# Performance work log

Measured on AMD Instinct MI355X. Metric: run time of the kernel, lower is better.

The kernel has to match this reference:

```python
import jax, jax.numpy as jnp
import numpy as np

D_MODEL = 1024
NUM_HEADS = 16
D_K = D_MODEL // NUM_HEADS


def setup_inputs() -> dict:
    key = jax.random.key(0)
    ks = jax.random.split(key, 11)
    B, S, D = 2, 2048, D_MODEL
    scale = 1.0 / np.sqrt(D)
    inp = {
        'q': jax.random.normal(ks[0], (B, S, D), jnp.float32),
        'k': jax.random.normal(ks[1], (B, S, D), jnp.float32),
        'v': jax.random.normal(ks[2], (B, S, D), jnp.float32),
        'wq': jax.random.normal(ks[3], (D, D), jnp.float32) * scale,
        'bq': jnp.zeros((D,), jnp.float32),
        'wk': jax.random.normal(ks[4], (D, D), jnp.float32) * scale,
        'bk': jnp.zeros((D,), jnp.float32),
        'wv': jax.random.normal(ks[5], (D, D), jnp.float32) * scale,
        'bv': jnp.zeros((D,), jnp.float32),
        'wo': jax.random.normal(ks[6], (D, D), jnp.float32) * scale,
        'bo': jnp.zeros((D,), jnp.float32),
    }
    return inp


def _split_heads(x):
    B, S, _ = x.shape
    return x.reshape(B, S, NUM_HEADS, D_K).transpose(0, 2, 1, 3)  # [B,H,S,dk]


def reference(q, k, v, wq, bq, wk, bk, wv, bv, wo, bo):
    # Linear projections (torch Linear: x @ W^T + b)
    qh = _split_heads(q @ wq.T + bq)
    kh = _split_heads(k @ wk.T + bk)
    vh = _split_heads(v @ wv.T + bv)
    scores = jnp.einsum('bhqd,bhkd->bhqk', qh, kh) / np.sqrt(D_K)
    attn = jax.nn.softmax(scores, axis=-1)  # dropout is identity in eval
    ctx = jnp.einsum('bhqk,bhkd->bhqd', attn, vh)
    B, H, S, dk = ctx.shape
    ctx = ctx.transpose(0, 2, 1, 3).reshape(B, S, H * dk)
    return ctx @ wo.T + bo
```

## Files before the change

kernel.cpp:

```cpp
#include <hip/hip_runtime.h>
#include <hip/hip_bf16.h>
#include <math.h>

#define BATCH 2
#define SEQ   2048
#define DMODEL 1024
#define NHEAD 16
#define DK    64
#define M_TOT (BATCH*SEQ)
#define KDIM  DMODEL

typedef short bf16x8 __attribute__((ext_vector_type(8)));
typedef short bf16x4 __attribute__((ext_vector_type(4)));
typedef float f32x4  __attribute__((ext_vector_type(4)));
typedef __hip_bfloat16 bf16;

#define QSCALE 0.18033688011112042f

__device__ inline void gld_lds16(const void* g, void* l) {
    __builtin_amdgcn_global_load_lds(
        (const __attribute__((address_space(1))) unsigned int*)g,
        (__attribute__((address_space(3))) unsigned int*)l, 16, 0, 0);
}

__device__ inline unsigned pack2(float a, float b) {
    union { __hip_bfloat162 h; unsigned u; } t;
    t.h = __float22bfloat162_rn(make_float2(a, b));
    return t.u;
}

__global__ __launch_bounds__(256) void conv_all(
    const float* __restrict__ q, const float* __restrict__ k, const float* __restrict__ v,
    const float* __restrict__ wq, const float* __restrict__ wk,
    const float* __restrict__ wv, const float* __restrict__ wo,
    bf16* __restrict__ qh, bf16* __restrict__ kh, bf16* __restrict__ vh,
    bf16* __restrict__ wqh, bf16* __restrict__ wkh, bf16* __restrict__ wvh,
    bf16* __restrict__ woh)
{
    const int y = blockIdx.y;
    const int i = (blockIdx.x * 256 + threadIdx.x) * 4;
    if (y < 3) {
        const float* src = y == 0 ? q : (y == 1 ? k : v);
        bf16* dst = y == 0 ? qh : (y == 1 ? kh : vh);
        float4 t = *(const float4*)(src + i);
        uint2 o;
        o.x = pack2(t.x, t.y);
        o.y = pack2(t.z, t.w);
        *(uint2*)(dst + i) = o;
    } else {
        const int w = i >> 20;
        const int j = i & ((1 << 20) - 1);
        const float* src = w == 0 ? wq : (w == 1 ? wk : (w == 2 ? wv : wo));
        bf16* dsth = w == 0 ? wqh : (w == 1 ? wkh : (w == 2 ? wvh : woh));
        float4 t = *(const float4*)(src + j);
        uint2 oh;
        oh.x = pack2(t.x, t.y);
        oh.y = pack2(t.z, t.w);
        *(uint2*)(dsth + j) = oh;
    }
}

__device__ __forceinline__ void gemm_body(
    const bf16* __restrict__ Ah, const bf16* __restrict__ Wh,
    const float* __restrict__ bias, void* __restrict__ out,
    int layout, float scale, bf16* sA, bf16* sB, int kb, int ke)
{
    const int tid  = threadIdx.x;
    const int wave = tid >> 6, lane = tid & 63;
    const int ln   = lane & 15, quad = lane >> 4;
    const int wm   = wave >> 1, wn = wave & 1;
    const int row0 = blockIdx.y * 128, col0 = blockIdx.x * 128;

    const int srow = lane >> 2;
    const int clog = (lane & 3) ^ (srow & 3);
    const size_t gA0 = (size_t)(row0 + wave * 16 + srow) * KDIM + clog * 8;
    const size_t gB0 = (size_t)(col0 + wave * 16 + srow) * KDIM + clog * 8;
    const int ldsoff = (wave * 16 + srow) * 64 + (lane & 3) * 16;

    const int swz = (quad ^ (ln & 3)) * 8;

    f32x4 acc[4][4] = {};

    for (int k0 = kb; k0 < ke; k0 += 32) {
        __syncthreads();
#pragma unroll
        for (int j = 0; j < 2; ++j) {
            const size_t go = (size_t)k0 + (size_t)j * 64 * KDIM;
            gld_lds16(Ah + gA0 + go, (char*)sA + j * 4096 + ldsoff);
            gld_lds16(Wh + gB0 + go, (char*)sB + j * 4096 + ldsoff);
        }
        __syncthreads();

        bf16x8 af[4], bfr[4];
#pragma unroll
        for (int t = 0; t < 4; ++t) {
            af[t]  = *(const bf16x8*)&sA[(wm * 64 + t * 16 + ln) * 32 + swz];
            bfr[t] = *(const bf16x8*)&sB[(wn * 64 + t * 16 + ln) * 32 + swz];
        }
#pragma unroll
        for (int mt = 0; mt < 4; ++mt)
#pragma unroll
            for (int nt = 0; nt < 4; ++nt)
                acc[mt][nt] = __builtin_amdgcn_mfma_f32_16x16x32_bf16(af[mt], bfr[nt], acc[mt][nt], 0, 0, 0);
    }

#pragma unroll
    for (int nt = 0; nt < 4; ++nt) {
        const int n = col0 + wn * 64 + nt * 16 + ln;
        const float bv = (layout == 3) ? 0.f : bias[n];
#pragma unroll
        for (int mt = 0; mt < 4; ++mt) {
#pragma unroll
            for (int r = 0; r < 4; ++r) {
                const int m = row0 + wm * 64 + mt * 16 + quad * 4 + r;
                const float v = (acc[mt][nt][r] + bv) * scale;
                if (layout == 0 || layout == 3) {
                    ((float*)out)[(size_t)m * DMODEL + n] = v;
                } else {
                    const int b = m >> 11, s = m & (SEQ - 1);
                    const int h = n >> 6,  d = n & (DK - 1);
                    const int bh = b * NHEAD + h;
                    bf16 hv = __float2bfloat16(v);
                    if (layout == 1)
                        ((bf16*)out)[((size_t)bh * SEQ + s) * DK + d] = hv;
                    else
                        ((bf16*)out)[((size_t)bh * DK + d) * SEQ + s] = hv;
                }
            }
        }
    }
}

struct QKVArgs {
    const bf16* A[3];
    const bf16* W[3];
    const float* bias[3];
    bf16* out[3];
    float scale[3];
    int layout[3];
};

__global__ __launch_bounds__(256) void qkv_gemm(QKVArgs a) {
    __shared__ __align__(16) bf16 sA[128 * 32];
    __shared__ __align__(16) bf16 sB[128 * 32];
    const int z = blockIdx.z;
    gemm_body(a.A[z], a.W[z], a.bias[z],
              (void*)a.out[z], a.layout[z], a.scale[z], sA, sB, 0, KDIM);
}

__global__ __launch_bounds__(256) void gemm_o(
    const bf16* __restrict__ Ah, const bf16* __restrict__ Wh,
    float* __restrict__ p0, float* __restrict__ p1)
{
    __shared__ __align__(16) bf16 sA[128 * 32];
    __shared__ __align__(16) bf16 sB[128 * 32];
    const int z = blockIdx.z;
    gemm_body(Ah, Wh, nullptr, (void*)(z ? p1 : p0), 3, 1.0f,
              sA, sB, z * (KDIM / 2), (z + 1) * (KDIM / 2));
}

__global__ __launch_bounds__(256) void combine_o(
    const float* __restrict__ p0, const float* __restrict__ p1,
    const float* __restrict__ bias, float* __restrict__ out)
{
    const int i = (blockIdx.x * 256 + threadIdx.x) * 4;
    float4 a = *(const float4*)(p0 + i);
    float4 b = *(const float4*)(p1 + i);
    float4 c = *(const float4*)(bias + (i & (DMODEL - 1)));
    float4 o;
    o.x = a.x + b.x + c.x;
    o.y = a.y + b.y + c.y;
    o.z = a.z + b.z + c.z;
    o.w = a.w + b.w + c.w;
    *(float4*)(out + i) = o;
}

#define NKT (SEQ / 64)
__global__ __launch_bounds__(256) void flash_attn_mfma(
    const bf16* __restrict__ Q, const bf16* __restrict__ K,
    const bf16* __restrict__ Vt, bf16* __restrict__ ctxh)
{
    __shared__ __align__(16) bf16 Vts[64 * 64];

    const int tid  = threadIdx.x;
    const int wave = tid >> 6, lane = tid & 63;
    const int ln   = lane & 15, quad = lane >> 4;
    const int qt   = blockIdx.x;
    const int bh   = blockIdx.y;
    const int b    = bh >> 4, h = bh & (NHEAD - 1);

    const int q0 = qt * 128 + wave * 32;
    const bf16* Qb = Q + ((size_t)bh * SEQ + q0) * DK;
    bf16x8 qf[2][2];
#pragma unroll
    for (int c = 0; c < 2; ++c)
#pragma unroll
        for (int nt = 0; nt < 2; ++nt)
            qf[c][nt] = *(const bf16x8*)(Qb + (size_t)(nt * 16 + ln) * DK + c * 32 + quad * 8);

    f32x4 of[2][4] = {};
    float lp[2] = {0.f, 0.f};

    const int sr  = tid >> 2;
    const int scb = (tid & 3) * 2;
    const int ssw = sr & 7;
    const bf16* Vg0 = Vt + ((size_t)bh * DK + sr) * SEQ;
    const bf16* Kl  = K + (size_t)bh * SEQ * DK + (size_t)ln * DK + quad * 8;

    int vaddr[4];
#pragma unroll
    for (int mt = 0; mt < 4; ++mt)
        vaddr[mt] = ln * 64 + (((2 * mt + (quad >> 1)) ^ (ln & 7)) * 8) + (quad & 1) * 4;

    bf16x8 kfA[2][4], kfB[2][4];
#pragma unroll
    for (int c = 0; c < 2; ++c)
#pragma unroll
        for (int mt = 0; mt < 4; ++mt)
            kfA[c][mt] = *(const bf16x8*)(Kl + (size_t)(mt * 16) * DK + c * 32);

    auto halfiter = [&](int ktc, bf16x8 (&kfc)[2][4], bf16x8 (&kfn)[2][4]) {
        __syncthreads();
        {
            const bf16* Vg = Vg0 + ktc * 64;
            uint4 v0 = *(const uint4*)(Vg + scb * 8);
            uint4 v1 = *(const uint4*)(Vg + scb * 8 + 8);
            *(uint4*)(&Vts[sr * 64 + ((scb    ) ^ ssw) * 8]) = v0;
            *(uint4*)(&Vts[sr * 64 + ((scb + 1) ^ ssw) * 8]) = v1;
        }
        __syncthreads();

        const int ktn = (ktc + 1) & (NKT - 1);
#pragma unroll
        for (int c = 0; c < 2; ++c)
#pragma unroll
            for (int mt = 0; mt < 4; ++mt)
                kfn[c][mt] = *(const bf16x8*)(Kl + (size_t)(ktn * 64 + mt * 16) * DK + c * 32);

        f32x4 st[4][2] = {};
#pragma unroll
        for (int c = 0; c < 2; ++c)
#pragma unroll
            for (int mt = 0; mt < 4; ++mt)
#pragma unroll
                for (int nt = 0; nt < 2; ++nt)
                    st[mt][nt] = __builtin_amdgcn_mfma_f32_16x16x32_bf16(kfc[c][mt], qf[c][nt], st[mt][nt], 0, 0, 0);

        bf16x4 aP[4][2];
#pragma unroll
        for (int mt = 0; mt < 4; ++mt)
#pragma unroll
            for (int nt = 0; nt < 2; ++nt) {
                float p0 = __builtin_amdgcn_exp2f(st[mt][nt][0]);
                float p1 = __builtin_amdgcn_exp2f(st[mt][nt][1]);
                float p2 = __builtin_amdgcn_exp2f(st[mt][nt][2]);
                float p3 = __builtin_amdgcn_exp2f(st[mt][nt][3]);
                lp[nt] += (p0 + p1) + (p2 + p3);
                union { bf16x4 v; uint2 u; } uu;
                uu.u.x = pack2(p0, p1);
                uu.u.y = pack2(p2, p3);
                aP[mt][nt] = uu.v;
            }

#pragma unroll
        for (int mt = 0; mt < 4; ++mt)
#pragma unroll
            for (int nt = 0; nt < 4; ++nt) {
                bf16x4 vf = *(const bf16x4*)(&Vts[vaddr[mt] + nt * 1024]);
                of[0][nt] = __builtin_amdgcn_mfma_f32_16x16x16bf16_1k(aP[mt][0], vf, of[0][nt], 0, 0, 0);
                of[1][nt] = __builtin_amdgcn_mfma_f32_16x16x16bf16_1k(aP[mt][1], vf, of[1][nt], 0, 0, 0);
            }
    };

    for (int kt = 0; kt < NKT; kt += 2) {
        halfiter(kt,     kfA, kfB);
        halfiter(kt + 1, kfB, kfA);
    }

#pragma unroll
    for (int nt = 0; nt < 2; ++nt) {
        lp[nt] += __shfl_xor(lp[nt], 16, 64);
        lp[nt] += __shfl_xor(lp[nt], 32, 64);
    }
    float linv[2][4];
#pragma unroll
    for (int mtP = 0; mtP < 2; ++mtP)
#pragma unroll
        for (int r = 0; r < 4; ++r)
            linv[mtP][r] = 1.0f / __shfl(lp[mtP], quad * 4 + r, 64);

    const size_t base = ((size_t)b * SEQ + q0) * DMODEL + h * DK;
#pragma unroll
    for (int mtP = 0; mtP < 2; ++mtP)
#pragma unroll
        for (int nt = 0; nt < 4; ++nt)
#pragma unroll
            for (int r = 0; r < 4; ++r) {
                const float v = of[mtP][nt][r] * linv[mtP][r];
                const size_t idx = base + (size_t)(mtP * 16 + quad * 4 + r) * DMODEL + nt * 16 + ln;
                ctxh[idx] = __float2bfloat16(v);
            }
}

extern "C" void kernel_launch(void* const* d_in, const int* in_sizes, int n_in,
                              void* d_out, int out_size, void* d_ws, size_t ws_size,
                              hipStream_t stream) {
    const float* q  = (const float*)d_in[0];
    const float* k  = (const float*)d_in[1];
    const float* v  = (const float*)d_in[2];
    const float* wq = (const float*)d_in[3];
    const float* bq = (const float*)d_in[4];
    const float* wk = (const float*)d_in[5];
    const float* bk = (const float*)d_in[6];
    const float* wv = (const float*)d_in[7];
    const float* bv = (const float*)d_in[8];
    const float* wo = (const float*)d_in[9];
    const float* bo = (const float*)d_in[10];
    float* out = (float*)d_out;

    char* ws = (char*)d_ws;
    const size_t MB = 1u << 20;
    bf16* wq_hi = (bf16*)(ws + 0 * MB);
    bf16* wk_hi = (bf16*)(ws + 2 * MB);
    bf16* wv_hi = (bf16*)(ws + 4 * MB);
    bf16* wo_hi = (bf16*)(ws + 6 * MB);
    bf16* q_hi  = (bf16*)(ws + 8 * MB);
    bf16* k_hi  = (bf16*)(ws + 16 * MB);
    bf16* v_hi  = (bf16*)(ws + 24 * MB);
    bf16* Qp    = (bf16*)(ws + 32 * MB);
    bf16* Kp    = (bf16*)(ws + 40 * MB);
    bf16* Vpt   = (bf16*)(ws + 48 * MB);
    bf16* ctx_h = (bf16*)(ws + 8 * MB);
    float* p0   = (float*)(ws + 16 * MB);
    float* p1   = (float*)(ws + 32 * MB);

    const int NX = M_TOT * DMODEL;

    conv_all<<<dim3(NX / 1024, 4), 256, 0, stream>>>(
        q, k, v, wq, wk, wv, wo,
        q_hi, k_hi, v_hi, wq_hi, wk_hi, wv_hi, wo_hi);

    QKVArgs qa;
    qa.A[0] = q_hi;  qa.A[1] = k_hi;  qa.A[2] = v_hi;
    qa.W[0] = wq_hi; qa.W[1] = wk_hi; qa.W[2] = wv_hi;
    qa.bias[0] = bq; qa.bias[1] = bk; qa.bias[2] = bv;
    qa.out[0] = Qp;  qa.out[1] = Kp;  qa.out[2] = Vpt;
    qa.scale[0] = QSCALE; qa.scale[1] = 1.0f; qa.scale[2] = 1.0f;
    qa.layout[0] = 1; qa.layout[1] = 1; qa.layout[2] = 2;

    dim3 qgrid(DMODEL / 128, M_TOT / 128, 3);
    qkv_gemm<<<qgrid, 256, 0, stream>>>(qa);

    dim3 fgrid(SEQ / 128, BATCH * NHEAD);
    flash_attn_mfma<<<fgrid, 256, 0, stream>>>(Qp, Kp, Vpt, ctx_h);

    dim3 ogrid(DMODEL / 128, M_TOT / 128, 2);
    gemm_o<<<ogrid, 256, 0, stream>>>(ctx_h, wo_hi, p0, p1);

    combine_o<<<NX / 1024, 256, 0, stream>>>(p0, p1, bo, out);
}
```

Measured before the change: 262.9 us.

## Split flash-attention KV range across two wave groups per block

The attention block grows from 256 to 512 threads, and two groups of four waves each process half of the key/value tiles for the same 128 queries. Each group has its own V tile in shared memory. Partial outputs and row sums are merged through shared memory at the end. This doubles the waves per block to raise occupancy and hide latency, since the grid has only 512 blocks. The cost is extra LDS for the merge buffers, one more barrier, and group 0 doing the final combine alone.

```diff
diff --git a/kernel.cpp b/kernel.cpp
--- a/kernel.cpp
+++ b/kernel.cpp
@@ -176,20 +176,24 @@
 }
 
 #define NKT (SEQ / 64)
-__global__ __launch_bounds__(256) void flash_attn_mfma(
+__global__ __launch_bounds__(512, 4) void flash_attn_mfma(
     const bf16* __restrict__ Q, const bf16* __restrict__ K,
     const bf16* __restrict__ Vt, bf16* __restrict__ ctxh)
 {
-    __shared__ __align__(16) bf16 Vts[64 * 64];
+    __shared__ __align__(16) bf16 Vts[2][64 * 64];
+    __shared__ __align__(16) float comb[4][32 * 68];
+    __shared__ float lpc[4][32];
 
     const int tid  = threadIdx.x;
     const int wave = tid >> 6, lane = tid & 63;
     const int ln   = lane & 15, quad = lane >> 4;
+    const int grp  = wave >> 2;
+    const int wv4  = wave & 3;
     const int qt   = blockIdx.x;
     const int bh   = blockIdx.y;
     const int b    = bh >> 4, h = bh & (NHEAD - 1);
 
-    const int q0 = qt * 128 + wave * 32;
+    const int q0 = qt * 128 + wv4 * 32;
     const bf16* Qb = Q + ((size_t)bh * SEQ + q0) * DK;
     bf16x8 qf[2][2];
 #pragma unroll
@@ -201,36 +205,42 @@
     f32x4 of[2][4] = {};
     float lp[2] = {0.f, 0.f};
 
-    const int sr  = tid >> 2;
-    const int scb = (tid & 3) * 2;
+    const int t4  = tid & 255;
+    const int sr  = t4 >> 2;
+    const int scb = (t4 & 3) * 2;
     const int ssw = sr & 7;
     const bf16* Vg0 = Vt + ((size_t)bh * DK + sr) * SEQ;
     const bf16* Kl  = K + (size_t)bh * SEQ * DK + (size_t)ln * DK + quad * 8;
+    const int kvb = grp * (NKT / 2);
+
+    bf16* VtsF = &Vts[0][0];
 
     int vaddr[4];
 #pragma unroll
     for (int mt = 0; mt < 4; ++mt)
-        vaddr[mt] = ln * 64 + (((2 * mt + (quad >> 1)) ^ (ln & 7)) * 8) + (quad & 1) * 4;
+        vaddr[mt] = grp * 4096 + ln * 64 + (((2 * mt + (quad >> 1)) ^ (ln & 7)) * 8) + (quad & 1) * 4;
 
     bf16x8 kfA[2][4], kfB[2][4];
 #pragma unroll
     for (int c = 0; c < 2; ++c)
 #pragma unroll
         for (int mt = 0; mt < 4; ++mt)
-            kfA[c][mt] = *(const bf16x8*)(Kl + (size_t)(mt * 16) * DK + c * 32);
-
-    auto halfiter = [&](int ktc, bf16x8 (&kfc)[2][4], bf16x8 (&kfn)[2][4]) {
+            kfA[c][mt] = *(const bf16x8*)(Kl + (size_t)(kvb * 64 + mt * 16) * DK + c * 32);
+
+    auto halfiter = [&](int ktl, bf16x8 (&kfc)[2][4], bf16x8 (&kfn)[2][4]) {
+        const int ktc = kvb + ktl;
         __syncthreads();
         {
             const bf16* Vg = Vg0 + ktc * 64;
             uint4 v0 = *(const uint4*)(Vg + scb * 8);
             uint4 v1 = *(const uint4*)(Vg + scb * 8 + 8);
-            *(uint4*)(&Vts[sr * 64 + ((scb    ) ^ ssw) * 8]) = v0;
-            *(uint4*)(&Vts[sr * 64 + ((scb + 1) ^ ssw) * 8]) = v1;
+            bf16* vd = &Vts[grp][sr * 64];
+            *(uint4*)(vd + ((scb    ) ^ ssw) * 8) = v0;
+            *(uint4*)(vd + ((scb + 1) ^ ssw) * 8) = v1;
         }
         __syncthreads();
 
-        const int ktn = (ktc + 1) & (NKT - 1);
+        const int ktn = kvb + ((ktl + 1) & (NKT / 2 - 1));
 #pragma unroll
         for (int c = 0; c < 2; ++c)
 #pragma unroll
@@ -266,15 +276,15 @@
         for (int mt = 0; mt < 4; ++mt)
 #pragma unroll
             for (int nt = 0; nt < 4; ++nt) {
-                bf16x4 vf = *(const bf16x4*)(&Vts[vaddr[mt] + nt * 1024]);
+                bf16x4 vf = *(const bf16x4*)(VtsF + vaddr[mt] + nt * 1024);
                 of[0][nt] = __builtin_amdgcn_mfma_f32_16x16x16bf16_1k(aP[mt][0], vf, of[0][nt], 0, 0, 0);
                 of[1][nt] = __builtin_amdgcn_mfma_f32_16x16x16bf16_1k(aP[mt][1], vf, of[1][nt], 0, 0, 0);
             }
     };
 
-    for (int kt = 0; kt < NKT; kt += 2) {
-        halfiter(kt,     kfA, kfB);
-        halfiter(kt + 1, kfB, kfA);
+    for (int ktl = 0; ktl < NKT / 2; ktl += 2) {
+        halfiter(ktl,     kfA, kfB);
+        halfiter(ktl + 1, kfB, kfA);
     }
 
 #pragma unroll
@@ -282,24 +292,51 @@
         lp[nt] += __shfl_xor(lp[nt], 16, 64);
         lp[nt] += __shfl_xor(lp[nt], 32, 64);
     }
-    float linv[2][4];
-#pragma unroll
-    for (int mtP = 0; mtP < 2; ++mtP)
-#pragma unroll
-        for (int r = 0; r < 4; ++r)
-            linv[mtP][r] = 1.0f / __shfl(lp[mtP], quad * 4 + r, 64);
-
-    const size_t base = ((size_t)b * SEQ + q0) * DMODEL + h * DK;
-#pragma unroll
-    for (int mtP = 0; mtP < 2; ++mtP)
-#pragma unroll
-        for (int nt = 0; nt < 4; ++nt)
-#pragma unroll
-            for (int r = 0; r < 4; ++r) {
-                const float v = of[mtP][nt][r] * linv[mtP][r];
-                const size_t idx = base + (size_t)(mtP * 16 + quad * 4 + r) * DMODEL + nt * 16 + ln;
-                ctxh[idx] = __float2bfloat16(v);
-            }
+
+    if (grp) {
+#pragma unroll
+        for (int mtP = 0; mtP < 2; ++mtP)
+#pragma unroll
+            for (int nt = 0; nt < 4; ++nt)
+#pragma unroll
+                for (int r = 0; r < 4; ++r)
+                    comb[wv4][(mtP * 16 + quad * 4 + r) * 68 + nt * 16 + ln] = of[mtP][nt][r];
+        if (quad == 0) {
+            lpc[wv4][ln]      = lp[0];
+            lpc[wv4][16 + ln] = lp[1];
+        }
+    }
+    __syncthreads();
+    if (!grp) {
+#pragma unroll
+        for (int mtP = 0; mtP < 2; ++mtP)
+#pragma unroll
+            for (int nt = 0; nt < 4; ++nt)
+#pragma unroll
+                for (int r = 0; r < 4; ++r)
+                    of[mtP][nt][r] += comb[wv4][(mtP * 16 + quad * 4 + r) * 68 + nt * 16 + ln];
+        lp[0] += lpc[wv4][ln];
+        lp[1] += lpc[wv4][16 + ln];
+
+        float linv[2][4];
+#pragma unroll
+        for (int mtP = 0; mtP < 2; ++mtP)
+#pragma unroll
+            for (int r = 0; r < 4; ++r)
+                linv[mtP][r] = 1.0f / __shfl(lp[mtP], quad * 4 + r, 64);
+
+        const size_t base = ((size_t)b * SEQ + q0) * DMODEL + h * DK;
+#pragma unroll
+        for (int mtP = 0; mtP < 2; ++mtP)
+#pragma unroll
+            for (int nt = 0; nt < 4; ++nt)
+#pragma unroll
+                for (int r = 0; r < 4; ++r) {
+                    const float v = of[mtP][nt][r] * linv[mtP][r];
+                    const size_t idx = base + (size_t)(mtP * 16 + quad * 4 + r) * DMODEL + nt * 16 + ln;
+                    ctxh[idx] = __float2bfloat16(v);
+                }
+    }
 }
 
 extern "C" void kernel_launch(void* const* d_in, const int* in_sizes, int n_in,
@@ -352,7 +389,7 @@
     qkv_gemm<<<qgrid, 256, 0, stream>>>(qa);
 
     dim3 fgrid(SEQ / 128, BATCH * NHEAD);
-    flash_attn_mfma<<<fgrid, 256, 0, stream>>>(Qp, Kp, Vpt, ctx_h);
+    flash_attn_mfma<<<fgrid, 512, 0, stream>>>(Qp, Kp, Vpt, ctx_h);
 
     dim3 ogrid(DMODEL / 128, M_TOT / 128, 2);
     gemm_o<<<ogrid, 256, 0, stream>>>(ctx_h, wo_hi, p0, p1);
```

New measurement: 331.4 us. 1.26x slower.
